# Kernel tuning notes

Measured on AMD Instinct MI355X. Metric: run time of the kernel, lower is better.

Reference implementation:

```python
import jax, jax.numpy as jnp
import numpy as np

INPUT, HIDDEN, OUTPUT = 512, 1024, 512

def setup_inputs() -> dict:
    key = jax.random.key(0)
    ks = jax.random.split(key, 6)
    s_i = 1.0 / np.sqrt(INPUT)
    s_h = 1.0 / np.sqrt(HIDDEN)
    return {
        "x": jax.random.normal(ks[0], (64, 512, INPUT), dtype=jnp.float32),
        "Wi": jax.random.normal(ks[1], (INPUT, HIDDEN), dtype=jnp.float32) * s_i,
        "bi": jax.random.normal(ks[2], (HIDDEN,), dtype=jnp.float32) * 0.01,
        "Wh": jax.random.normal(ks[3], (HIDDEN, HIDDEN), dtype=jnp.float32) * s_h,
        "Wo": jax.random.normal(ks[4], (HIDDEN, OUTPUT), dtype=jnp.float32) * s_h,
        "bo": jax.random.normal(ks[5], (OUTPUT,), dtype=jnp.float32) * 0.01,
    }

def reference(x, Wi, bi, Wh, Wo, bo):
    B, S, _ = x.shape
    # Precompute input projection for all timesteps: [B,S,H]
    xi = jnp.einsum("bsi,ih->bsh", x, Wi) + bi
    h0 = jnp.zeros((B, Wh.shape[0]), dtype=x.dtype)

    def scan_fn(h, xi_t):
        # flax SimpleCell: tanh(dense_i(x) + dense_h(h)); module applies relu on top
        h_next = jax.nn.relu(jnp.tanh(xi_t + h @ Wh))
        return h_next, h_next

    _, h_stacked = jax.lax.scan(scan_fn, h0, jnp.transpose(xi, (1, 0, 2)))  # [S,B,H]
    h_stacked = jnp.transpose(h_stacked, (1, 0, 2))  # [B,S,H]
    y = jnp.einsum("bsh,ho->bso", h_stacked, Wo) + bo
    return y
```

## Files before the change

kernel.cpp:

```cpp
#include <hip/hip_runtime.h>
#include <math.h>

#define BATCH   64
#define SEQ     512
#define NIN     512
#define NHID    1024
#define NOUT    512

typedef short short8 __attribute__((ext_vector_type(8)));
typedef float f32x4 __attribute__((ext_vector_type(4)));

__device__ __forceinline__ unsigned short f2bf(float f) {
  unsigned int u = __float_as_uint(f);
  unsigned int r = (u + 0x7fffu + ((u >> 16) & 1u)) >> 16;
  return (unsigned short)r;
}

#define GROUPS 8
#define BPG    32
#define BPERG  8

#define FMA4(hv, wv4, accv)              \
  accv.x = fmaf(hv, wv4.x, accv.x);      \
  accv.y = fmaf(hv, wv4.y, accv.y);      \
  accv.z = fmaf(hv, wv4.z, accv.z);      \
  accv.w = fmaf(hv, wv4.w, accv.w);

#define BM 128
#define BN 64
#define BK 16

__global__ __launch_bounds__(256) void gemm_bias(
    const float* __restrict__ A, const float* __restrict__ B,
    const float* __restrict__ bias, float* __restrict__ C,
    int M, int N, int K) {
  __shared__ float As[BK][BM + 4];
  __shared__ float Bs[BK][BN + 4];

  const int tid = threadIdx.x;
  const int bx = blockIdx.x;
  const int by = blockIdx.y;

  const int tm = (tid / 16) * 8;
  const int tn = (tid % 16) * 4;

  const int ar = tid / 4;
  const int ac = (tid % 4) * 4;
  const int br = tid / 16;
  const int bc = (tid % 16) * 4;

  float acc[8][4] = {};

  for (int k0 = 0; k0 < K; k0 += BK) {
    float4 av0 = *(const float4*)&A[(size_t)(by * BM + ar) * K + k0 + ac];
    float4 av1 = *(const float4*)&A[(size_t)(by * BM + ar + 64) * K + k0 + ac];
    As[ac + 0][ar] = av0.x;  As[ac + 0][ar + 64] = av1.x;
    As[ac + 1][ar] = av0.y;  As[ac + 1][ar + 64] = av1.y;
    As[ac + 2][ar] = av0.z;  As[ac + 2][ar + 64] = av1.z;
    As[ac + 3][ar] = av0.w;  As[ac + 3][ar + 64] = av1.w;
    float4 bv = *(const float4*)&B[(size_t)(k0 + br) * N + bx * BN + bc];
    *(float4*)&Bs[br][bc] = bv;
    __syncthreads();

#pragma unroll
    for (int k = 0; k < BK; ++k) {
      float4 a0 = *(const float4*)&As[k][tm];
      float4 a1 = *(const float4*)&As[k][tm + 4];
      float4 b4 = *(const float4*)&Bs[k][tn];
      float ae[8] = {a0.x, a0.y, a0.z, a0.w, a1.x, a1.y, a1.z, a1.w};
      float be[4] = {b4.x, b4.y, b4.z, b4.w};
#pragma unroll
      for (int i = 0; i < 8; ++i)
#pragma unroll
        for (int j = 0; j < 4; ++j)
          acc[i][j] = fmaf(ae[i], be[j], acc[i][j]);
    }
    __syncthreads();
  }

  const float4 bb = *(const float4*)&bias[bx * BN + tn];
#pragma unroll
  for (int i = 0; i < 8; ++i) {
    float4 o;
    o.x = acc[i][0] + bb.x;
    o.y = acc[i][1] + bb.y;
    o.z = acc[i][2] + bb.z;
    o.w = acc[i][3] + bb.w;
    *(float4*)&C[(size_t)(by * BM + tm + i) * N + bx * BN + tn] = o;
  }
}

#define OBM 128
#define OBN 128
#define OBK 32
#define LDK 40

__global__ __launch_bounds__(256) void gemm_bias_bf16(
    const float* __restrict__ A, const float* __restrict__ B,
    const float* __restrict__ bias, float* __restrict__ C,
    int M, int N, int K) {
  __shared__ unsigned short Asb[OBM][LDK];
  __shared__ unsigned short Bsb[OBN][LDK];

  const int tid  = threadIdx.x;
  const int lane = tid & 63;
  const int wid  = tid >> 6;
  const int wm   = wid >> 1;
  const int wn   = wid & 1;
  const int bx   = blockIdx.x;
  const int by   = blockIdx.y;

  const int ar  = tid >> 1;
  const int aks = (tid & 1) * 16;
  const int bk4 = (tid >> 5) * 4;
  const int bn4 = (tid & 31) * 4;

  const int l15 = lane & 15;
  const int lk8 = (lane >> 4) * 8;

  f32x4 acc[4][4];
#pragma unroll
  for (int i = 0; i < 4; ++i)
#pragma unroll
    for (int j = 0; j < 4; ++j) acc[i][j] = (f32x4){0.f, 0.f, 0.f, 0.f};

  for (int k0 = 0; k0 < K; k0 += OBK) {
    const float* Ap = &A[(size_t)(by * OBM + ar) * K + k0 + aks];
    float4 a0 = *(const float4*)(Ap + 0);
    float4 a1 = *(const float4*)(Ap + 4);
    float4 a2 = *(const float4*)(Ap + 8);
    float4 a3 = *(const float4*)(Ap + 12);
    unsigned short ta[16] = {
        f2bf(a0.x), f2bf(a0.y), f2bf(a0.z), f2bf(a0.w),
        f2bf(a1.x), f2bf(a1.y), f2bf(a1.z), f2bf(a1.w),
        f2bf(a2.x), f2bf(a2.y), f2bf(a2.z), f2bf(a2.w),
        f2bf(a3.x), f2bf(a3.y), f2bf(a3.z), f2bf(a3.w)};
    *(short8*)&Asb[ar][aks + 0] = *(short8*)&ta[0];
    *(short8*)&Asb[ar][aks + 8] = *(short8*)&ta[8];

#pragma unroll
    for (int kk = 0; kk < 4; ++kk) {
      float4 bv = *(const float4*)&B[(size_t)(k0 + bk4 + kk) * N + bx * OBN + bn4];
      Bsb[bn4 + 0][bk4 + kk] = f2bf(bv.x);
      Bsb[bn4 + 1][bk4 + kk] = f2bf(bv.y);
      Bsb[bn4 + 2][bk4 + kk] = f2bf(bv.z);
      Bsb[bn4 + 3][bk4 + kk] = f2bf(bv.w);
    }
    __syncthreads();

    short8 afr[4], bfr[4];
#pragma unroll
    for (int t = 0; t < 4; ++t) {
      afr[t] = *(const short8*)&Asb[wm * 64 + t * 16 + l15][lk8];
      bfr[t] = *(const short8*)&Bsb[wn * 64 + t * 16 + l15][lk8];
    }
#pragma unroll
    for (int rt = 0; rt < 4; ++rt)
#pragma unroll
      for (int ct = 0; ct < 4; ++ct)
        acc[rt][ct] = __builtin_amdgcn_mfma_f32_16x16x32_bf16(
            afr[rt], bfr[ct], acc[rt][ct], 0, 0, 0);
    __syncthreads();
  }

#pragma unroll
  for (int rt = 0; rt < 4; ++rt) {
    const int row0 = by * OBM + wm * 64 + rt * 16 + (lane >> 4) * 4;
#pragma unroll
    for (int ct = 0; ct < 4; ++ct) {
      const int col = bx * OBN + wn * 64 + ct * 16 + l15;
      const float bb = bias[col];
#pragma unroll
      for (int i = 0; i < 4; ++i)
        C[(size_t)(row0 + i) * N + col] = acc[rt][ct][i] + bb;
    }
  }
}

__global__ __launch_bounds__(256, 1) void rnn_scan_ws(
    const float* __restrict__ Wh, float* __restrict__ xi,
    unsigned int* flags) {
  __shared__ float hs[BPERG * NHID];
  __shared__ float P[256 * 32];

  const int tid  = threadIdx.x;
  const int bg   = blockIdx.x & 7;
  const int jc   = blockIdx.x >> 3;
  const int c4   = tid & 7;
  const int kseg = tid >> 3;
  const int colbase = jc * 32 + c4 * 4;
  const int hswz  = (kseg & 7) << 2;
  const int stswz = ((tid >> 3) & 7) << 2;
  const int ob   = tid >> 5;
  const int ocol = tid & 31;
  const int oc4  = ocol >> 2;
  const int oce  = ocol & 3;

  float4 w[32];
#pragma unroll
  for (int kk = 0; kk < 32; ++kk)
    w[kk] = *(const float4*)&Wh[(size_t)(kseg * 32 + kk) * NHID + colbase];

  float* const xrow_base =
      xi + (size_t)(bg * BPERG + ob) * SEQ * NHID + jc * 32 + ocol;
  unsigned int* const gflags = flags + bg * 32;
  unsigned int* const myflag = gflags + jc;
  unsigned int* const pollflag = gflags + (tid & 31);

  float xin = __hip_atomic_load(xrow_base, __ATOMIC_RELAXED,
                                __HIP_MEMORY_SCOPE_AGENT);

  for (int s = 0; s < SEQ; ++s) {
    float* prow = xrow_base + (size_t)s * NHID;

    float4 acc[BPERG];
#pragma unroll
    for (int b = 0; b < BPERG; ++b) acc[b] = make_float4(0.f, 0.f, 0.f, 0.f);

    if (s > 0) {
      const float* base =
          xi + (size_t)(bg * BPERG) * SEQ * NHID + (size_t)(s - 1) * NHID + tid * 4;
#pragma unroll
      for (int b = 0; b < BPERG; ++b) {
        float4 v = *(const float4*)(base + (size_t)b * SEQ * NHID);
        *(float4*)&hs[b * NHID + ((tid * 4) ^ stswz)] = v;
      }
      __syncthreads();

#pragma unroll
      for (int b = 0; b < BPERG; ++b) {
#pragma unroll
        for (int kq = 0; kq < 8; ++kq) {
          const float4 h4 =
              *(const float4*)&hs[b * NHID + kseg * 32 + ((kq * 4) ^ hswz)];
          FMA4(h4.x, w[kq * 4 + 0], acc[b]);
          FMA4(h4.y, w[kq * 4 + 1], acc[b]);
          FMA4(h4.z, w[kq * 4 + 2], acc[b]);
          FMA4(h4.w, w[kq * 4 + 3], acc[b]);
        }
      }
    }

    {
      const int u = kseg * 8 + c4;
      const int sw = (((kseg & 7) ^ c4)) << 2;
#pragma unroll
      for (int b = 0; b < BPERG; ++b)
        *(float4*)&P[u * 32 + ((b * 4) ^ sw)] = acc[b];
    }
    __syncthreads();

    float sum = 0.f;
#pragma unroll
    for (int q = 0; q < 32; ++q) {
      const int uu = q * 8 + oc4;
      const int sw2 = ((q & 7) ^ oc4) << 2;
      sum += P[uu * 32 + ((ob * 4 + oce) ^ sw2)];
    }

    const float hn = fmaxf(tanhf(xin + sum), 0.f);
    __hip_atomic_store(prow, hn, __ATOMIC_RELAXED, __HIP_MEMORY_SCOPE_AGENT);

    __syncthreads();
    const unsigned int target = (unsigned int)(s + 1);
    if (tid == 0)
      __hip_atomic_store(myflag, target, __ATOMIC_RELAXED,
                         __HIP_MEMORY_SCOPE_AGENT);

    if (s + 1 < SEQ)
      xin = __hip_atomic_load(xrow_base + (size_t)(s + 1) * NHID,
                              __ATOMIC_RELAXED, __HIP_MEMORY_SCOPE_AGENT);

    if (tid < 64) {
      while (true) {
        unsigned int v = __hip_atomic_load(pollflag, __ATOMIC_RELAXED,
                                           __HIP_MEMORY_SCOPE_AGENT);
        if (__all(v >= target)) break;
        __builtin_amdgcn_s_sleep(1);
      }
    }
    __syncthreads();
  }
}

__global__ __launch_bounds__(256, 2) void rnn_fused(
    const float* __restrict__ Wh, const float* __restrict__ Wi,
    const float* __restrict__ x, const float* __restrict__ bi,
    float* __restrict__ xi, unsigned int* flags) {
  __shared__ float smem[16384];
  const int tid = threadIdx.x;
  unsigned int* const xi_done = flags + 256;

  if (blockIdx.x >= GROUPS * BPG) {
    const int bw = blockIdx.x - GROUPS * BPG;
    float* As = smem;
    float* Bs = smem + 16 * 132;
    const int tm = (tid / 16) * 8;
    const int tn = (tid % 16) * 4;
    const int ar = tid / 4;
    const int ac = (tid % 4) * 4;
    const int br = tid / 16;
    const int bc = (tid % 16) * 4;
    const int b0 = ar >> 1;
    const int so = ar & 1;

    for (int i = 0; i < 16; ++i) {
      const int j = (i << 8) + bw;
      const int st = j >> 4;
      const int ct = j & 15;
      const int s2 = 2 * st + so;

      float acc[8][4] = {};
      for (int k0 = 0; k0 < NIN; k0 += 16) {
        float4 av0 = *(const float4*)&x[((size_t)b0 * SEQ + s2) * NIN + k0 + ac];
        float4 av1 =
            *(const float4*)&x[((size_t)(b0 + 32) * SEQ + s2) * NIN + k0 + ac];
        As[(ac + 0) * 132 + ar] = av0.x;  As[(ac + 0) * 132 + ar + 64] = av1.x;
        As[(ac + 1) * 132 + ar] = av0.y;  As[(ac + 1) * 132 + ar + 64] = av1.y;
        As[(ac + 2) * 132 + ar] = av0.z;  As[(ac + 2) * 132 + ar + 64] = av1.z;
        As[(ac + 3) * 132 + ar] = av0.w;  As[(ac + 3) * 132 + ar + 64] = av1.w;
        float4 bv = *(const float4*)&Wi[(size_t)(k0 + br) * NHID + ct * 64 + bc];
        *(float4*)&Bs[br * 68 + bc] = bv;
        __syncthreads();

#pragma unroll
        for (int k = 0; k < 16; ++k) {
          float4 a0 = *(const float4*)&As[k * 132 + tm];
          float4 a1 = *(const float4*)&As[k * 132 + tm + 4];
          float4 b4 = *(const float4*)&Bs[k * 68 + tn];
          float ae[8] = {a0.x, a0.y, a0.z, a0.w, a1.x, a1.y, a1.z, a1.w};
          float be[4] = {b4.x, b4.y, b4.z, b4.w};
#pragma unroll
          for (int ii = 0; ii < 8; ++ii)
#pragma unroll
            for (int jj = 0; jj < 4; ++jj)
              acc[ii][jj] = fmaf(ae[ii], be[jj], acc[ii][jj]);
        }
        __syncthreads();
      }

      const float4 bb = *(const float4*)&bi[ct * 64 + tn];
#pragma unroll
      for (int r = 0; r < 8; ++r) {
        const int row = tm + r;
        const int b = row >> 1;
        const int s = 2 * st + (row & 1);
        f32x4 o;
        o[0] = acc[r][0] + bb.x;
        o[1] = acc[r][1] + bb.y;
        o[2] = acc[r][2] + bb.z;
        o[3] = acc[r][3] + bb.w;
        float* cp = xi + ((size_t)b * SEQ + s) * NHID + ct * 64 + tn;
        asm volatile("global_store_dwordx4 %0, %1, off sc0 sc1"
                     :: "v"(cp), "v"(o) : "memory");
      }
      asm volatile("s_waitcnt vmcnt(0)" ::: "memory");
      __builtin_amdgcn_sched_barrier(0);
      __syncthreads();
      if (tid == 0) atomicAdd(&xi_done[st], 1u);
      __syncthreads();
    }
    return;
  }

  __builtin_amdgcn_s_setprio(1);
  float* hs = smem;
  float* P  = smem + 8192;

  const int bg   = blockIdx.x & 7;
  const int jc   = blockIdx.x >> 3;
  const int c4   = tid & 7;
  const int kseg = tid >> 3;
  const int colbase = jc * 32 + c4 * 4;
  const int hswz  = (kseg & 7) << 2;
  const int stswz = ((tid >> 3) & 7) << 2;
  const int ob   = tid >> 5;
  const int ocol = tid & 31;
  const int oc4  = ocol >> 2;
  const int oce  = ocol & 3;

  float4 w[32];
#pragma unroll
  for (int kk = 0; kk < 32; ++kk)
    w[kk] = *(const float4*)&Wh[(size_t)(kseg * 32 + kk) * NHID + colbase];

  float* const xrow_base =
      xi + (size_t)(bg * BPERG + ob) * SEQ * NHID + jc * 32 + ocol;
  unsigned int* const gflags = flags + bg * 32;
  unsigned int* const myflag = gflags + jc;

  if (tid < 64) {
    while (__hip_atomic_load(xi_done, __ATOMIC_RELAXED,
                             __HIP_MEMORY_SCOPE_AGENT) < 16u)
      __builtin_amdgcn_s_sleep(1);
  }
  __syncthreads();

  for (int s = 0; s < SEQ; ++s) {
    float* prow = xrow_base + (size_t)s * NHID;
    const float xin = __hip_atomic_load(prow, __ATOMIC_RELAXED,
                                        __HIP_MEMORY_SCOPE_AGENT);

    float4 acc[BPERG];
#pragma unroll
    for (int b = 0; b < BPERG; ++b) acc[b] = make_float4(0.f, 0.f, 0.f, 0.f);

    if (s > 0) {
      const float* base =
          xi + (size_t)(bg * BPERG) * SEQ * NHID + (size_t)(s - 1) * NHID + tid * 4;
#pragma unroll
      for (int b = 0; b < BPERG; ++b) {
        float4 v = *(const float4*)(base + (size_t)b * SEQ * NHID);
        *(float4*)&hs[b * NHID + ((tid * 4) ^ stswz)] = v;
      }
      __syncthreads();

#pragma unroll
      for (int b = 0; b < BPERG; ++b) {
#pragma unroll
        for (int kq = 0; kq < 8; ++kq) {
          const float4 h4 =
              *(const float4*)&hs[b * NHID + kseg * 32 + ((kq * 4) ^ hswz)];
          FMA4(h4.x, w[kq * 4 + 0], acc[b]);
          FMA4(h4.y, w[kq * 4 + 1], acc[b]);
          FMA4(h4.z, w[kq * 4 + 2], acc[b]);
          FMA4(h4.w, w[kq * 4 + 3], acc[b]);
        }
      }
    }

    {
      const int u = kseg * 8 + c4;
      const int sw = (((kseg & 7) ^ c4)) << 2;
#pragma unroll
      for (int b = 0; b < BPERG; ++b)
        *(float4*)&P[u * 32 + ((b * 4) ^ sw)] = acc[b];
    }
    __syncthreads();

    float sum = 0.f;
#pragma unroll
    for (int q = 0; q < 32; ++q) {
      const int uu = q * 8 + oc4;
      const int sw2 = ((q & 7) ^ oc4) << 2;
      sum += P[uu * 32 + ((ob * 4 + oce) ^ sw2)];
    }

    const float hn = fmaxf(tanhf(xin + sum), 0.f);
    __hip_atomic_store(prow, hn, __ATOMIC_RELAXED, __HIP_MEMORY_SCOPE_AGENT);

    __syncthreads();
    const unsigned int target = (unsigned int)(s + 1);
    if (tid == 0)
      __hip_atomic_store(myflag, target, __ATOMIC_RELAXED,
                         __HIP_MEMORY_SCOPE_AGENT);

    if (tid < 64) {
      const int nxt = s + 1;
      const int tile = (nxt < SEQ) ? (nxt >> 1) : 0;
      const unsigned int thr =
          (tid < 32) ? target : ((nxt < SEQ) ? 16u : 0u);
      const unsigned int* pp =
          (tid < 32) ? (gflags + tid) : (xi_done + tile);
      while (true) {
        unsigned int v = __hip_atomic_load(pp, __ATOMIC_RELAXED,
                                           __HIP_MEMORY_SCOPE_AGENT);
        if (__all(v >= thr)) break;
        __builtin_amdgcn_s_sleep(1);
      }
    }
    __syncthreads();
  }
}

extern "C" void kernel_launch(void* const* d_in, const int* in_sizes, int n_in,
                              void* d_out, int out_size, void* d_ws, size_t ws_size,
                              hipStream_t stream) {
  const float* x  = (const float*)d_in[0];
  const float* Wi = (const float*)d_in[1];
  const float* bi = (const float*)d_in[2];
  const float* Wh = (const float*)d_in[3];
  const float* Wo = (const float*)d_in[4];
  const float* bo = (const float*)d_in[5];
  float* out = (float*)d_out;
  float* xi  = (float*)d_ws;

  unsigned int* flags = (unsigned int*)d_out;

  const int M = BATCH * SEQ;

  dim3 blk(256);
  hipMemsetAsync(flags, 0, 2048, stream);

  int occ = 0;
  hipError_t qerr = hipOccupancyMaxActiveBlocksPerMultiprocessor(
      &occ, (const void*)rnn_fused, 256, 0);
  bool fused_ok = (qerr == hipSuccess) && (occ >= 2);

  if (fused_ok) {
    const float* Wh_p = Wh;
    const float* Wi_p = Wi;
    const float* x_p  = x;
    const float* bi_p = bi;
    float* xi_p = xi;
    unsigned int* flags_p = flags;
    void* args[6] = {(void*)&Wh_p, (void*)&Wi_p, (void*)&x_p,
                     (void*)&bi_p, (void*)&xi_p, (void*)&flags_p};
    hipError_t err = hipLaunchCooperativeKernel(
        (const void*)rnn_fused, dim3(GROUPS * BPG + 256), dim3(256), args, 0,
        stream);
    fused_ok = (err == hipSuccess);
  }

  if (!fused_ok) {
    gemm_bias<<<dim3(NHID / BN, M / BM), blk, 0, stream>>>(x, Wi, bi, xi, M,
                                                           NHID, NIN);
    const float* Wh_p = Wh;
    float* xi_p = xi;
    unsigned int* flags_p = flags;
    void* args[3] = {(void*)&Wh_p, (void*)&xi_p, (void*)&flags_p};
    hipLaunchCooperativeKernel((const void*)rnn_scan_ws, dim3(GROUPS * BPG),
                               dim3(256), args, 0, stream);
  }

  gemm_bias_bf16<<<dim3(NOUT / OBN, M / OBM), blk, 0, stream>>>(xi, Wo, bo, out,
                                                               M, NOUT, NHID);
}
```

Baseline: 2.467 ms.

## Throttle xi producer blocks on recurrence progress and restructure B-tile staging

The output GEMM's B-tile load switches from float4 loads with strided 16-bit LDS scatters to scalar coalesced loads. Pairs of bf16 values are packed into 32-bit LDS stores. In the persistent recurrence kernel, the xi-precompute worker blocks now wait on the recurrence groups' progress flags before each later chunk. This throttles the producers so they do not run too far ahead or compete for bandwidth and CUs with the latency-critical recurrence. The throttling adds spin-wait overhead and a deadlock risk if the flag thresholds are wrong.

```diff
diff --git a/kernel.cpp b/kernel.cpp
--- a/kernel.cpp
+++ b/kernel.cpp
@@ -113,7 +113,7 @@
   const int ar  = tid >> 1;
   const int aks = (tid & 1) * 16;
   const int bk4 = (tid >> 5) * 4;
-  const int bn4 = (tid & 31) * 4;
+  const int tb  = tid & 31;
 
   const int l15 = lane & 15;
   const int lk8 = (lane >> 4) * 8;
@@ -138,14 +138,21 @@
     *(short8*)&Asb[ar][aks + 0] = *(short8*)&ta[0];
     *(short8*)&Asb[ar][aks + 8] = *(short8*)&ta[8];
 
-#pragma unroll
-    for (int kk = 0; kk < 4; ++kk) {
-      float4 bv = *(const float4*)&B[(size_t)(k0 + bk4 + kk) * N + bx * OBN + bn4];
-      Bsb[bn4 + 0][bk4 + kk] = f2bf(bv.x);
-      Bsb[bn4 + 1][bk4 + kk] = f2bf(bv.y);
-      Bsb[bn4 + 2][bk4 + kk] = f2bf(bv.z);
-      Bsb[bn4 + 3][bk4 + kk] = f2bf(bv.w);
-    }
+    float bvv[4][4];
+#pragma unroll
+    for (int kk = 0; kk < 4; ++kk)
+#pragma unroll
+      for (int jj = 0; jj < 4; ++jj)
+        bvv[kk][jj] =
+            B[(size_t)(k0 + bk4 + kk) * N + bx * OBN + jj * 32 + tb];
+#pragma unroll
+    for (int jj = 0; jj < 4; ++jj)
+#pragma unroll
+      for (int kk = 0; kk < 4; kk += 2) {
+        unsigned int pk = (unsigned int)f2bf(bvv[kk][jj]) |
+                          ((unsigned int)f2bf(bvv[kk + 1][jj]) << 16);
+        *(unsigned int*)&Bsb[jj * 32 + tb][bk4 + kk] = pk;
+      }
     __syncthreads();
 
     short8 afr[4], bfr[4];
@@ -305,6 +312,20 @@
     const int so = ar & 1;
 
     for (int i = 0; i < 16; ++i) {
+      if (i >= 3) {
+        const unsigned int thr = (unsigned int)(32 * (i - 2));
+        if (tid < 64) {
+          const unsigned int* pf = flags + ((tid & 7) << 5);
+          while (true) {
+            unsigned int v = __hip_atomic_load(pf, __ATOMIC_RELAXED,
+                                               __HIP_MEMORY_SCOPE_AGENT);
+            if (__all(v >= thr)) break;
+            __builtin_amdgcn_s_sleep(32);
+          }
+        }
+        __syncthreads();
+      }
+
       const int j = (i << 8) + bw;
       const int st = j >> 4;
       const int ct = j & 15;
```

New measurement: 2.414 ms. 2.1% less time.
